# Optimization experiments

Hardware: AMD Instinct MI355X
Metric: run time of the kernel (lower is better)

The kernel has to match this reference:

```python
import jax, jax.numpy as jnp
import numpy as np
from jax import lax

H = 32  # hidden size


def _lstm_layer(x, Wih, Whh, bih, bhh):
    """x: [B, T, D_in]; returns [B, T, H]. PyTorch gate order i,f,g,o."""
    B = x.shape[0]
    b = bih + bhh  # [4H]
    # precompute input projections for all timesteps: [T, B, 4H]
    xp = jnp.einsum('btd,gd->tbg', x, Wih) + b

    def step(carry, xt):
        h, c = carry
        gates = xt + h @ Whh.T  # [B, 4H]
        i, f, g, o = jnp.split(gates, 4, axis=-1)
        i = jax.nn.sigmoid(i)
        f = jax.nn.sigmoid(f)
        g = jnp.tanh(g)
        o = jax.nn.sigmoid(o)
        c = f * c + i * g
        h = o * jnp.tanh(c)
        return (h, c), h

    init = (jnp.zeros((B, H), x.dtype), jnp.zeros((B, H), x.dtype))
    _, ys = lax.scan(step, init, xp)  # ys: [T, B, H]
    return jnp.swapaxes(ys, 0, 1)


def _lstm5(x, Wih0, Wih_rest, Whh, bih, bhh):
    h = _lstm_layer(x, Wih0, Whh[0], bih[0], bhh[0])
    for l in range(4):  # fixed small layer count
        h = _lstm_layer(h, Wih_rest[l], Whh[l + 1], bih[l + 1], bhh[l + 1])
    return h


def setup_inputs() -> dict:
    key = jax.random.key(0)
    ks = jax.random.split(key, 18)
    s = 1.0 / np.sqrt(H)
    B, T = 16384, 20
    u = lambda k, shp: jax.random.uniform(k, shp, jnp.float32, -s, s)
    return {
        'accel': jax.random.normal(ks[0], (B, T, 3), jnp.float32),
        'gyro': jax.random.normal(ks[1], (B, T, 3), jnp.float32),
        'accel_Wih0': u(ks[2], (4 * H, 3)),
        'accel_Wih_rest': u(ks[3], (4, 4 * H, H)),
        'accel_Whh': u(ks[4], (5, 4 * H, H)),
        'accel_bih': u(ks[5], (5, 4 * H)),
        'accel_bhh': u(ks[6], (5, 4 * H)),
        'gyro_Wih0': u(ks[7], (4 * H, 3)),
        'gyro_Wih_rest': u(ks[8], (4, 4 * H, H)),
        'gyro_Whh': u(ks[9], (5, 4 * H, H)),
        'gyro_bih': u(ks[10], (5, 4 * H)),
        'gyro_bhh': u(ks[11], (5, 4 * H)),
        'fc1_w': u(ks[12], (128, T * H * 2)),
        'fc1_b': u(ks[13], (128,)),
        'fc2_w': u(ks[14], (5, 128)),
        'fc2_b': u(ks[15], (5,)),
    }


def reference(accel, gyro, accel_Wih0, accel_Wih_rest, accel_Whh, accel_bih,
              accel_bhh, gyro_Wih0, gyro_Wih_rest, gyro_Whh, gyro_bih,
              gyro_bhh, fc1_w, fc1_b, fc2_w, fc2_b):
    a = _lstm5(accel, accel_Wih0, accel_Wih_rest, accel_Whh, accel_bih, accel_bhh)
    g = _lstm5(gyro, gyro_Wih0, gyro_Wih_rest, gyro_Whh, gyro_bih, gyro_bhh)
    x = jnp.concatenate([a, g], axis=1)          # [B, 2T, H]
    x = x.reshape(x.shape[0], -1)                # [B, 2*T*H]
    x = jax.nn.relu(x @ fc1_w.T + fc1_b)         # [B, 128]
    return x @ fc2_w.T + fc2_b                   # [B, 5]
```

## Files before the change

kernel.cpp:

```cpp
#include <hip/hip_runtime.h>
#include <math.h>

#define B_TOTAL 16384
#define T_STEPS 20
#define NGRP    1024

typedef __attribute__((ext_vector_type(8))) __bf16 bf16x8;
typedef __attribute__((ext_vector_type(4))) float f32x4;

__device__ __forceinline__ float sigf(float x) {
    return __builtin_amdgcn_rcpf(1.0f + __expf(-x));
}
__device__ __forceinline__ float tanhf_fast(float x) {
    return fmaf(-2.0f, __builtin_amdgcn_rcpf(__expf(2.0f * x) + 1.0f), 1.0f);
}

__device__ __forceinline__ __bf16 bf16_bits(unsigned short s) {
    __bf16 r; __builtin_memcpy(&r, &s, 2); return r;
}
__device__ __forceinline__ void split_trunc(float x, __bf16& hi, __bf16& lo) {
    unsigned u = __float_as_uint(x);
    hi = bf16_bits((unsigned short)(u >> 16));
    float l = x - __uint_as_float(u & 0xFFFF0000u);
    lo = bf16_bits((unsigned short)(__float_as_uint(l) >> 16));
}

__global__ __launch_bounds__(256, 4)
void lstm5_mfma(const float* __restrict__ accel, const float* __restrict__ gyro,
                const float* __restrict__ aWih0, const float* __restrict__ aWihR,
                const float* __restrict__ aWhh,  const float* __restrict__ aBih,
                const float* __restrict__ aBhh,
                const float* __restrict__ gWih0, const float* __restrict__ gWihR,
                const float* __restrict__ gWhh,  const float* __restrict__ gBih,
                const float* __restrict__ gBhh,
                __bf16* __restrict__ Xhi, __bf16* __restrict__ Xlo) {
    const int tid  = threadIdx.x;
    const int w    = tid >> 6;
    const int lane = tid & 63;
    const int e    = lane & 15;
    const int quad = lane >> 4;
    const int sensor = blockIdx.y;
    const int bbase  = blockIdx.x * 16;

    const float* xin  = sensor ? gyro  : accel;
    const float* Wih0 = sensor ? gWih0 : aWih0;
    const float* WihR = sensor ? gWihR : aWihR;
    const float* Whh  = sensor ? gWhh  : aWhh;
    const float* Bih  = sensor ? gBih  : aBih;
    const float* Bhh  = sensor ? gBhh  : aBhh;

    __shared__ __align__(16) __bf16 shi[20 * 512];
    __shared__ __align__(16) __bf16 slo[20 * 512];

    const int ug0 = w * 8 + quad;
    const int ug1 = w * 8 + 4 + quad;

    const int m_row   = lane & 15;
    const int orow_t0 = (m_row & 3) * 32 + (w * 8 + (m_row >> 2));
    const int orow_t1 = (m_row & 3) * 32 + (w * 8 + 4 + (m_row >> 2));

    bf16x8 wih_h0, wih_l0, wih_h1, wih_l1;
    bf16x8 whh_h0, whh_l0, whh_h1, whh_l1;
    f32x4  bias0v, bias1v;
    float  c0 = 0.f, c1 = 0.f;

#define LOAD_FRAG(Wsrc, orow, fh, fl)                         \
    {                                                         \
        const float* p_ = (Wsrc) + (orow) * 32 + quad * 8;    \
        _Pragma("unroll")                                     \
        for (int jj = 0; jj < 8; ++jj) {                      \
            __bf16 h_, l_;                                    \
            split_trunc(p_[jj], h_, l_);                      \
            (fh)[jj] = h_;  (fl)[jj] = l_;                    \
        }                                                     \
    }

#define LOAD_BIAS(l)                                                        \
    {                                                                       \
        _Pragma("unroll")                                                   \
        for (int r = 0; r < 4; ++r) {                                       \
            bias0v[r] = Bih[(l) * 128 + r * 32 + ug0] + Bhh[(l) * 128 + r * 32 + ug0]; \
            bias1v[r] = Bih[(l) * 128 + r * 32 + ug1] + Bhh[(l) * 128 + r * 32 + ug1]; \
        }                                                                   \
    }

#define ACT_STORE(t)                                                        \
    {                                                                       \
        float i0 = sigf(acc0[0]), f0 = sigf(acc0[1]);                       \
        float g0 = tanhf_fast(acc0[2]), o0 = sigf(acc0[3]);                 \
        c0 = f0 * c0 + i0 * g0;                                             \
        float h0 = o0 * tanhf_fast(c0);                                     \
        float i1 = sigf(acc1[0]), f1 = sigf(acc1[1]);                       \
        float g1 = tanhf_fast(acc1[2]), o1 = sigf(acc1[3]);                 \
        c1 = f1 * c1 + i1 * g1;                                             \
        float h1 = o1 * tanhf_fast(c1);                                     \
        __syncthreads();             \
        int i0x = (t) * 512 + w * 128 + e * 8 + quad;                       \
        int i1x = i0x + 4;                                                  \
        __bf16 hh_, ll_;                                                    \
        split_trunc(h0, hh_, ll_);  shi[i0x] = hh_;  slo[i0x] = ll_;        \
        split_trunc(h1, hh_, ll_);  shi[i1x] = hh_;  slo[i1x] = ll_;        \
        __syncthreads();       \
    }

    {
        LOAD_FRAG(Whh, orow_t0, whh_h0, whh_l0);
        LOAD_FRAG(Whh, orow_t1, whh_h1, whh_l1);
        LOAD_BIAS(0);
        float w0reg[2][4][3];
#pragma unroll
        for (int r = 0; r < 4; ++r)
#pragma unroll
            for (int k = 0; k < 3; ++k) {
                w0reg[0][r][k] = Wih0[(r * 32 + ug0) * 3 + k];
                w0reg[1][r][k] = Wih0[(r * 32 + ug1) * 3 + k];
            }
        const float* xrow = xin + (size_t)(bbase + e) * (T_STEPS * 3);

        for (int t = 0; t < T_STEPS; ++t) {
            float x0 = xrow[t * 3 + 0];
            float x1 = xrow[t * 3 + 1];
            float x2 = xrow[t * 3 + 2];
            f32x4 acc0 = bias0v;
            f32x4 acc1 = bias1v;
#pragma unroll
            for (int r = 0; r < 4; ++r) {
                acc0[r] = fmaf(w0reg[0][r][0], x0,
                          fmaf(w0reg[0][r][1], x1,
                          fmaf(w0reg[0][r][2], x2, acc0[r])));
                acc1[r] = fmaf(w0reg[1][r][0], x0,
                          fmaf(w0reg[1][r][1], x1,
                          fmaf(w0reg[1][r][2], x2, acc1[r])));
            }
            if (t > 0) {
                int rb = (t - 1) * 512 + quad * 128 + e * 8;
                bf16x8 bh = *(const bf16x8*)&shi[rb];
                bf16x8 bl = *(const bf16x8*)&slo[rb];
                acc0 = __builtin_amdgcn_mfma_f32_16x16x32_bf16(whh_h0, bh, acc0, 0, 0, 0);
                acc0 = __builtin_amdgcn_mfma_f32_16x16x32_bf16(whh_h0, bl, acc0, 0, 0, 0);
                acc0 = __builtin_amdgcn_mfma_f32_16x16x32_bf16(whh_l0, bh, acc0, 0, 0, 0);
                acc1 = __builtin_amdgcn_mfma_f32_16x16x32_bf16(whh_h1, bh, acc1, 0, 0, 0);
                acc1 = __builtin_amdgcn_mfma_f32_16x16x32_bf16(whh_h1, bl, acc1, 0, 0, 0);
                acc1 = __builtin_amdgcn_mfma_f32_16x16x32_bf16(whh_l1, bh, acc1, 0, 0, 0);
            }
            ACT_STORE(t);
        }
    }

    for (int l = 1; l < 5; ++l) {
        const float* Wi = WihR + (l - 1) * 4096;
        const float* Wh = Whh + l * 4096;
        LOAD_FRAG(Wi, orow_t0, wih_h0, wih_l0);
        LOAD_FRAG(Wi, orow_t1, wih_h1, wih_l1);
        LOAD_FRAG(Wh, orow_t0, whh_h0, whh_l0);
        LOAD_FRAG(Wh, orow_t1, whh_h1, whh_l1);
        LOAD_BIAS(l);
        c0 = 0.f; c1 = 0.f;

        for (int t = 0; t < T_STEPS; ++t) {
            f32x4 acc0, acc1;
            {
                int rb = t * 512 + quad * 128 + e * 8;
                bf16x8 bh = *(const bf16x8*)&shi[rb];
                bf16x8 bl = *(const bf16x8*)&slo[rb];
                acc0 = __builtin_amdgcn_mfma_f32_16x16x32_bf16(wih_h0, bh, bias0v, 0, 0, 0);
                acc0 = __builtin_amdgcn_mfma_f32_16x16x32_bf16(wih_h0, bl, acc0, 0, 0, 0);
                acc0 = __builtin_amdgcn_mfma_f32_16x16x32_bf16(wih_l0, bh, acc0, 0, 0, 0);
                acc1 = __builtin_amdgcn_mfma_f32_16x16x32_bf16(wih_h1, bh, bias1v, 0, 0, 0);
                acc1 = __builtin_amdgcn_mfma_f32_16x16x32_bf16(wih_h1, bl, acc1, 0, 0, 0);
                acc1 = __builtin_amdgcn_mfma_f32_16x16x32_bf16(wih_l1, bh, acc1, 0, 0, 0);
            }
            if (t > 0) {
                int rb = (t - 1) * 512 + quad * 128 + e * 8;
                bf16x8 bh = *(const bf16x8*)&shi[rb];
                bf16x8 bl = *(const bf16x8*)&slo[rb];
                acc0 = __builtin_amdgcn_mfma_f32_16x16x32_bf16(whh_h0, bh, acc0, 0, 0, 0);
                acc0 = __builtin_amdgcn_mfma_f32_16x16x32_bf16(whh_h0, bl, acc0, 0, 0, 0);
                acc0 = __builtin_amdgcn_mfma_f32_16x16x32_bf16(whh_l0, bh, acc0, 0, 0, 0);
                acc1 = __builtin_amdgcn_mfma_f32_16x16x32_bf16(whh_h1, bh, acc1, 0, 0, 0);
                acc1 = __builtin_amdgcn_mfma_f32_16x16x32_bf16(whh_h1, bl, acc1, 0, 0, 0);
                acc1 = __builtin_amdgcn_mfma_f32_16x16x32_bf16(whh_l1, bh, acc1, 0, 0, 0);
            }
            ACT_STORE(t);
        }
    }
    __syncthreads();

    {
        size_t base = ((size_t)(sensor * NGRP + blockIdx.x)) * (20 * 512);
        float4* dh = (float4*)(Xhi + base);
        float4* dl = (float4*)(Xlo + base);
        const float4* sh = (const float4*)shi;
        const float4* sl = (const float4*)slo;
        for (int i = tid; i < 20 * 512 / 8; i += 256) { dh[i] = sh[i]; dl[i] = sl[i]; }
    }
#undef LOAD_FRAG
#undef LOAD_BIAS
#undef ACT_STORE
}

__global__ void w1_prep(const float* __restrict__ w1,
                        __bf16* __restrict__ w1ah, __bf16* __restrict__ w1al) {
    int t = blockIdx.x * blockDim.x + threadIdx.x;
    if (t >= 20480) return;
    int lane = t & 63;
    int ks   = (t >> 6) % 40;
    int mt   = t / (64 * 40);
    int row  = mt * 16 + (lane & 15);
    int col0 = ks * 32 + (lane >> 4) * 8;
    const float* src = w1 + row * 1280 + col0;
#pragma unroll
    for (int j = 0; j < 8; ++j) {
        __bf16 h_, l_;
        split_trunc(src[j], h_, l_);
        w1ah[t * 8 + j] = h_;
        w1al[t * 8 + j] = l_;
    }
}

__global__ __launch_bounds__(256, 4)
void fc_mfma(const __bf16* __restrict__ Xhi, const __bf16* __restrict__ Xlo,
             const __bf16* __restrict__ w1ah, const __bf16* __restrict__ w1al,
             const float* __restrict__ fc1_b, const float* __restrict__ fc2_w,
             const float* __restrict__ fc2_b, float* __restrict__ out) {
    const int tid  = threadIdx.x;
    const int wv   = tid >> 6;
    const int lane = tid & 63;
    const int e    = lane & 15;
    const int quad = lane >> 4;
    const int g    = blockIdx.x;

    __shared__ __align__(16) f32x4 sacc[4][8][64];
    __shared__ float sred[4][16][5];

    f32x4 acc[8];
#pragma unroll
    for (int m = 0; m < 8; ++m) acc[m] = (f32x4){0.f, 0.f, 0.f, 0.f};

    for (int kk = 0; kk < 10; ++kk) {
        int ks = wv * 10 + kk;
        int sensor = ks / 20, t = ks % 20;
        size_t bb = ((size_t)(sensor * NGRP + g)) * (20 * 512) + t * 512 + lane * 8;
        bf16x8 bh = *(const bf16x8*)(Xhi + bb);
        bf16x8 bl = *(const bf16x8*)(Xlo + bb);
#pragma unroll
        for (int m = 0; m < 8; ++m) {
            const __bf16* ap = w1ah + ((size_t)((m * 40 + ks) * 64 + lane)) * 8;
            const __bf16* al = w1al + ((size_t)((m * 40 + ks) * 64 + lane)) * 8;
            bf16x8 ah = *(const bf16x8*)ap;
            bf16x8 av = *(const bf16x8*)al;
            acc[m] = __builtin_amdgcn_mfma_f32_16x16x32_bf16(ah, bh, acc[m], 0, 0, 0);
            acc[m] = __builtin_amdgcn_mfma_f32_16x16x32_bf16(ah, bl, acc[m], 0, 0, 0);
            acc[m] = __builtin_amdgcn_mfma_f32_16x16x32_bf16(av, bh, acc[m], 0, 0, 0);
        }
    }
#pragma unroll
    for (int m = 0; m < 8; ++m) sacc[wv][m][lane] = acc[m];
    __syncthreads();

    float p[5] = {0.f, 0.f, 0.f, 0.f, 0.f};
#pragma unroll
    for (int mm = 0; mm < 2; ++mm) {
        int mt = wv * 2 + mm;
        f32x4 z = sacc[0][mt][lane];
#pragma unroll
        for (int k = 1; k < 4; ++k) {
            f32x4 zz = sacc[k][mt][lane];
#pragma unroll
            for (int r = 0; r < 4; ++r) z[r] += zz[r];
        }
#pragma unroll
        for (int r = 0; r < 4; ++r) {
            int row = mt * 16 + quad * 4 + r;
            float v = fmaxf(z[r] + fc1_b[row], 0.f);
#pragma unroll
            for (int n = 0; n < 5; ++n) p[n] = fmaf(v, fc2_w[n * 128 + row], p[n]);
        }
    }
#pragma unroll
    for (int n = 0; n < 5; ++n) {
        p[n] += __shfl_xor(p[n], 16, 64);
        p[n] += __shfl_xor(p[n], 32, 64);
    }
    if (quad == 0) {
#pragma unroll
        for (int n = 0; n < 5; ++n) sred[wv][e][n] = p[n];
    }
    __syncthreads();
    if (tid < 80) {
        int col = tid / 5, n = tid - col * 5;
        out[(size_t)(g * 16 + col) * 5 + n] =
            sred[0][col][n] + sred[1][col][n] + sred[2][col][n] + sred[3][col][n] + fc2_b[n];
    }
}

extern "C" void kernel_launch(void* const* d_in, const int* in_sizes, int n_in,
                              void* d_out, int out_size, void* d_ws, size_t ws_size,
                              hipStream_t stream) {
    const float* accel  = (const float*)d_in[0];
    const float* gyro   = (const float*)d_in[1];
    const float* aWih0  = (const float*)d_in[2];
    const float* aWihR  = (const float*)d_in[3];
    const float* aWhh   = (const float*)d_in[4];
    const float* aBih   = (const float*)d_in[5];
    const float* aBhh   = (const float*)d_in[6];
    const float* gWih0  = (const float*)d_in[7];
    const float* gWihR  = (const float*)d_in[8];
    const float* gWhh   = (const float*)d_in[9];
    const float* gBih   = (const float*)d_in[10];
    const float* gBhh   = (const float*)d_in[11];
    const float* fc1_w  = (const float*)d_in[12];
    const float* fc1_b  = (const float*)d_in[13];
    const float* fc2_w  = (const float*)d_in[14];
    const float* fc2_b  = (const float*)d_in[15];
    float* out = (float*)d_out;

    const size_t XN = (size_t)2 * NGRP * 20 * 512;
    __bf16* Xhi  = (__bf16*)d_ws;
    __bf16* Xlo  = Xhi + XN;
    __bf16* W1ah = Xlo + XN;
    __bf16* W1al = W1ah + 163840;

    hipLaunchKernelGGL(w1_prep, dim3(80), dim3(256), 0, stream, fc1_w, W1ah, W1al);

    hipLaunchKernelGGL(lstm5_mfma, dim3(NGRP, 2), dim3(256), 0, stream,
                       accel, gyro, aWih0, aWihR, aWhh, aBih, aBhh,
                       gWih0, gWihR, gWhh, gBih, gBhh, Xhi, Xlo);

    hipLaunchKernelGGL(fc_mfma, dim3(NGRP), dim3(256), 0, stream,
                       Xhi, Xlo, W1ah, W1al, fc1_b, fc2_w, fc2_b, out);
}
```

Before: 294.4 us.

## Pack hidden-state stores with swizzled LDS layout, fuse gate math, batch FC groups

The activation math now shares the exponentials and reciprocals of all four gates, so each cell update uses two rcp calls instead of six. The hidden-state high/low bf16 values are packed as 32-bit words and written to an XOR-swizzled shared layout, with matching K-permutations in the weight fragments and the fc1 weight prep. This is meant to cut LDS store count and bank conflicts in the recurrent loop. The FC kernel now handles two batch groups per block, reusing each fc1 weight fragment load for twice as many MFMAs. The trade-offs are fewer FC blocks and a slightly different rounding path in the activations.

```diff
diff --git a/kernel.cpp b/kernel.cpp
--- a/kernel.cpp
+++ b/kernel.cpp
@@ -8,11 +8,12 @@
 typedef __attribute__((ext_vector_type(8))) __bf16 bf16x8;
 typedef __attribute__((ext_vector_type(4))) float f32x4;
 
-__device__ __forceinline__ float sigf(float x) {
-    return __builtin_amdgcn_rcpf(1.0f + __expf(-x));
-}
-__device__ __forceinline__ float tanhf_fast(float x) {
-    return fmaf(-2.0f, __builtin_amdgcn_rcpf(__expf(2.0f * x) + 1.0f), 1.0f);
+__device__ __forceinline__ unsigned pack_hi16(unsigned a, unsigned b) {
+#if __has_builtin(__builtin_amdgcn_perm)
+    return __builtin_amdgcn_perm(b, a, 0x07060302u);
+#else
+    return (a >> 16) | (b & 0xFFFF0000u);
+#endif
 }
 
 __device__ __forceinline__ __bf16 bf16_bits(unsigned short s) {
@@ -23,6 +24,20 @@
     hi = bf16_bits((unsigned short)(u >> 16));
     float l = x - __uint_as_float(u & 0xFFFF0000u);
     lo = bf16_bits((unsigned short)(__float_as_uint(l) >> 16));
+}
+
+__device__ __forceinline__ float lstm_act(f32x4 a, float& c) {
+    float eA = __expf(-a[0]);
+    float eB = __expf(-a[1]);
+    float eC = __expf(2.0f * a[2]);
+    float aA = 1.0f + eA, aB = 1.0f + eB, aC = 1.0f + eC;
+    float pAC = aA * aC;
+    float r1  = __builtin_amdgcn_rcpf(pAC * aB);
+    c = fmaf(c, pAC, (eC - 1.0f) * aB) * r1;
+    float eD = __expf(-a[3]);
+    float eE = __expf(2.0f * c);
+    float r2 = __builtin_amdgcn_rcpf((1.0f + eD) * (1.0f + eE));
+    return (eE - 1.0f) * r2;
 }
 
 __global__ __launch_bounds__(256, 4)
@@ -49,8 +64,13 @@
     const float* Bih  = sensor ? gBih  : aBih;
     const float* Bhh  = sensor ? gBhh  : aBhh;
 
-    __shared__ __align__(16) __bf16 shi[20 * 512];
-    __shared__ __align__(16) __bf16 slo[20 * 512];
+    __shared__ __align__(16) unsigned shi[20 * 256];
+    __shared__ __align__(16) unsigned slo[20 * 256];
+    const __bf16* sh16 = (const __bf16*)shi;
+    const __bf16* sl16 = (const __bf16*)slo;
+
+    const int wr_idx  = w * 64 + ((e * 4) ^ (w << 3)) + quad;
+    const int rb_base = quad * 128 + ((e * 8) ^ (quad << 4));
 
     const int ug0 = w * 8 + quad;
     const int ug1 = w * 8 + 4 + quad;
@@ -70,7 +90,7 @@
         _Pragma("unroll")                                     \
         for (int jj = 0; jj < 8; ++jj) {                      \
             __bf16 h_, l_;                                    \
-            split_trunc(p_[jj], h_, l_);                      \
+            split_trunc(p_[(jj >> 1) + ((jj & 1) << 2)], h_, l_); \
             (fh)[jj] = h_;  (fl)[jj] = l_;                    \
         }                                                     \
     }
@@ -86,20 +106,16 @@
 
 #define ACT_STORE(t)                                                        \
     {                                                                       \
-        float i0 = sigf(acc0[0]), f0 = sigf(acc0[1]);                       \
-        float g0 = tanhf_fast(acc0[2]), o0 = sigf(acc0[3]);                 \
-        c0 = f0 * c0 + i0 * g0;                                             \
-        float h0 = o0 * tanhf_fast(c0);                                     \
-        float i1 = sigf(acc1[0]), f1 = sigf(acc1[1]);                       \
-        float g1 = tanhf_fast(acc1[2]), o1 = sigf(acc1[3]);                 \
-        c1 = f1 * c1 + i1 * g1;                                             \
-        float h1 = o1 * tanhf_fast(c1);                                     \
+        float h0 = lstm_act(acc0, c0);                                      \
+        float h1 = lstm_act(acc1, c1);                                      \
+        unsigned b0 = __float_as_uint(h0), b1 = __float_as_uint(h1);        \
+        unsigned hp = pack_hi16(b0, b1);                                    \
+        float l0 = h0 - __uint_as_float(b0 & 0xFFFF0000u);                  \
+        float l1 = h1 - __uint_as_float(b1 & 0xFFFF0000u);                  \
+        unsigned lp = pack_hi16(__float_as_uint(l0), __float_as_uint(l1));  \
         __syncthreads();             \
-        int i0x = (t) * 512 + w * 128 + e * 8 + quad;                       \
-        int i1x = i0x + 4;                                                  \
-        __bf16 hh_, ll_;                                                    \
-        split_trunc(h0, hh_, ll_);  shi[i0x] = hh_;  slo[i0x] = ll_;        \
-        split_trunc(h1, hh_, ll_);  shi[i1x] = hh_;  slo[i1x] = ll_;        \
+        shi[(t) * 256 + wr_idx] = hp;                                       \
+        slo[(t) * 256 + wr_idx] = lp;                                       \
         __syncthreads();       \
     }
 
@@ -133,9 +149,9 @@
                           fmaf(w0reg[1][r][2], x2, acc1[r])));
             }
             if (t > 0) {
-                int rb = (t - 1) * 512 + quad * 128 + e * 8;
-                bf16x8 bh = *(const bf16x8*)&shi[rb];
-                bf16x8 bl = *(const bf16x8*)&slo[rb];
+                int rb = (t - 1) * 512 + rb_base;
+                bf16x8 bh = *(const bf16x8*)(sh16 + rb);
+                bf16x8 bl = *(const bf16x8*)(sl16 + rb);
                 acc0 = __builtin_amdgcn_mfma_f32_16x16x32_bf16(whh_h0, bh, acc0, 0, 0, 0);
                 acc0 = __builtin_amdgcn_mfma_f32_16x16x32_bf16(whh_h0, bl, acc0, 0, 0, 0);
                 acc0 = __builtin_amdgcn_mfma_f32_16x16x32_bf16(whh_l0, bh, acc0, 0, 0, 0);
@@ -158,22 +174,20 @@
         c0 = 0.f; c1 = 0.f;
 
         for (int t = 0; t < T_STEPS; ++t) {
+            const int rb1 = t * 512 + rb_base;
+            bf16x8 bh1 = *(const bf16x8*)(sh16 + rb1);
+            bf16x8 bl1 = *(const bf16x8*)(sl16 + rb1);
             f32x4 acc0, acc1;
-            {
-                int rb = t * 512 + quad * 128 + e * 8;
-                bf16x8 bh = *(const bf16x8*)&shi[rb];
-                bf16x8 bl = *(const bf16x8*)&slo[rb];
-                acc0 = __builtin_amdgcn_mfma_f32_16x16x32_bf16(wih_h0, bh, bias0v, 0, 0, 0);
-                acc0 = __builtin_amdgcn_mfma_f32_16x16x32_bf16(wih_h0, bl, acc0, 0, 0, 0);
-                acc0 = __builtin_amdgcn_mfma_f32_16x16x32_bf16(wih_l0, bh, acc0, 0, 0, 0);
-                acc1 = __builtin_amdgcn_mfma_f32_16x16x32_bf16(wih_h1, bh, bias1v, 0, 0, 0);
-                acc1 = __builtin_amdgcn_mfma_f32_16x16x32_bf16(wih_h1, bl, acc1, 0, 0, 0);
-                acc1 = __builtin_amdgcn_mfma_f32_16x16x32_bf16(wih_l1, bh, acc1, 0, 0, 0);
-            }
+            acc0 = __builtin_amdgcn_mfma_f32_16x16x32_bf16(wih_h0, bh1, bias0v, 0, 0, 0);
+            acc0 = __builtin_amdgcn_mfma_f32_16x16x32_bf16(wih_h0, bl1, acc0, 0, 0, 0);
+            acc0 = __builtin_amdgcn_mfma_f32_16x16x32_bf16(wih_l0, bh1, acc0, 0, 0, 0);
+            acc1 = __builtin_amdgcn_mfma_f32_16x16x32_bf16(wih_h1, bh1, bias1v, 0, 0, 0);
+            acc1 = __builtin_amdgcn_mfma_f32_16x16x32_bf16(wih_h1, bl1, acc1, 0, 0, 0);
+            acc1 = __builtin_amdgcn_mfma_f32_16x16x32_bf16(wih_l1, bh1, acc1, 0, 0, 0);
             if (t > 0) {
-                int rb = (t - 1) * 512 + quad * 128 + e * 8;
-                bf16x8 bh = *(const bf16x8*)&shi[rb];
-                bf16x8 bl = *(const bf16x8*)&slo[rb];
+                const int rb0 = rb1 - 512;
+                bf16x8 bh = *(const bf16x8*)(sh16 + rb0);
+                bf16x8 bl = *(const bf16x8*)(sl16 + rb0);
                 acc0 = __builtin_amdgcn_mfma_f32_16x16x32_bf16(whh_h0, bh, acc0, 0, 0, 0);
                 acc0 = __builtin_amdgcn_mfma_f32_16x16x32_bf16(whh_h0, bl, acc0, 0, 0, 0);
                 acc0 = __builtin_amdgcn_mfma_f32_16x16x32_bf16(whh_l0, bh, acc0, 0, 0, 0);
@@ -192,7 +206,7 @@
         float4* dl = (float4*)(Xlo + base);
         const float4* sh = (const float4*)shi;
         const float4* sl = (const float4*)slo;
-        for (int i = tid; i < 20 * 512 / 8; i += 256) { dh[i] = sh[i]; dl[i] = sl[i]; }
+        for (int i = tid; i < 1280; i += 256) { dh[i] = sh[i]; dl[i] = sl[i]; }
     }
 #undef LOAD_FRAG
 #undef LOAD_BIAS
@@ -212,7 +226,7 @@
 #pragma unroll
     for (int j = 0; j < 8; ++j) {
         __bf16 h_, l_;
-        split_trunc(src[j], h_, l_);
+        split_trunc(src[(j >> 1) + ((j & 1) << 2)], h_, l_);
         w1ah[t * 8 + j] = h_;
         w1al[t * 8 + j] = l_;
     }
@@ -228,69 +242,83 @@
     const int lane = tid & 63;
     const int e    = lane & 15;
     const int quad = lane >> 4;
-    const int g    = blockIdx.x;
+    const int g0   = blockIdx.x * 2;
+
+    const int lnoff = (lane * 8) ^ (quad << 4);
 
     __shared__ __align__(16) f32x4 sacc[4][8][64];
     __shared__ float sred[4][16][5];
 
-    f32x4 acc[8];
-#pragma unroll
-    for (int m = 0; m < 8; ++m) acc[m] = (f32x4){0.f, 0.f, 0.f, 0.f};
+    f32x4 acc[2][8];
+#pragma unroll
+    for (int p = 0; p < 2; ++p)
+#pragma unroll
+        for (int m = 0; m < 8; ++m) acc[p][m] = (f32x4){0.f, 0.f, 0.f, 0.f};
 
     for (int kk = 0; kk < 10; ++kk) {
         int ks = wv * 10 + kk;
         int sensor = ks / 20, t = ks % 20;
-        size_t bb = ((size_t)(sensor * NGRP + g)) * (20 * 512) + t * 512 + lane * 8;
-        bf16x8 bh = *(const bf16x8*)(Xhi + bb);
-        bf16x8 bl = *(const bf16x8*)(Xlo + bb);
+        size_t bb0 = ((size_t)(sensor * NGRP + g0)) * (20 * 512) + t * 512 + lnoff;
+        size_t bb1 = bb0 + (size_t)(20 * 512);
+        bf16x8 bh0 = *(const bf16x8*)(Xhi + bb0);
+        bf16x8 bl0 = *(const bf16x8*)(Xlo + bb0);
+        bf16x8 bh1 = *(const bf16x8*)(Xhi + bb1);
+        bf16x8 bl1 = *(const bf16x8*)(Xlo + bb1);
 #pragma unroll
         for (int m = 0; m < 8; ++m) {
             const __bf16* ap = w1ah + ((size_t)((m * 40 + ks) * 64 + lane)) * 8;
             const __bf16* al = w1al + ((size_t)((m * 40 + ks) * 64 + lane)) * 8;
             bf16x8 ah = *(const bf16x8*)ap;
             bf16x8 av = *(const bf16x8*)al;
-            acc[m] = __builtin_amdgcn_mfma_f32_16x16x32_bf16(ah, bh, acc[m], 0, 0, 0);
-            acc[m] = __builtin_amdgcn_mfma_f32_16x16x32_bf16(ah, bl, acc[m], 0, 0, 0);
-            acc[m] = __builtin_amdgcn_mfma_f32_16x16x32_bf16(av, bh, acc[m], 0, 0, 0);
-        }
-    }
-#pragma unroll
-    for (int m = 0; m < 8; ++m) sacc[wv][m][lane] = acc[m];
-    __syncthreads();
-
-    float p[5] = {0.f, 0.f, 0.f, 0.f, 0.f};
-#pragma unroll
-    for (int mm = 0; mm < 2; ++mm) {
-        int mt = wv * 2 + mm;
-        f32x4 z = sacc[0][mt][lane];
-#pragma unroll
-        for (int k = 1; k < 4; ++k) {
-            f32x4 zz = sacc[k][mt][lane];
-#pragma unroll
-            for (int r = 0; r < 4; ++r) z[r] += zz[r];
-        }
-#pragma unroll
-        for (int r = 0; r < 4; ++r) {
-            int row = mt * 16 + quad * 4 + r;
-            float v = fmaxf(z[r] + fc1_b[row], 0.f);
-#pragma unroll
-            for (int n = 0; n < 5; ++n) p[n] = fmaf(v, fc2_w[n * 128 + row], p[n]);
-        }
-    }
-#pragma unroll
-    for (int n = 0; n < 5; ++n) {
-        p[n] += __shfl_xor(p[n], 16, 64);
-        p[n] += __shfl_xor(p[n], 32, 64);
-    }
-    if (quad == 0) {
-#pragma unroll
-        for (int n = 0; n < 5; ++n) sred[wv][e][n] = p[n];
-    }
-    __syncthreads();
-    if (tid < 80) {
-        int col = tid / 5, n = tid - col * 5;
-        out[(size_t)(g * 16 + col) * 5 + n] =
-            sred[0][col][n] + sred[1][col][n] + sred[2][col][n] + sred[3][col][n] + fc2_b[n];
+            acc[0][m] = __builtin_amdgcn_mfma_f32_16x16x32_bf16(ah, bh0, acc[0][m], 0, 0, 0);
+            acc[0][m] = __builtin_amdgcn_mfma_f32_16x16x32_bf16(ah, bl0, acc[0][m], 0, 0, 0);
+            acc[0][m] = __builtin_amdgcn_mfma_f32_16x16x32_bf16(av, bh0, acc[0][m], 0, 0, 0);
+            acc[1][m] = __builtin_amdgcn_mfma_f32_16x16x32_bf16(ah, bh1, acc[1][m], 0, 0, 0);
+            acc[1][m] = __builtin_amdgcn_mfma_f32_16x16x32_bf16(ah, bl1, acc[1][m], 0, 0, 0);
+            acc[1][m] = __builtin_amdgcn_mfma_f32_16x16x32_bf16(av, bh1, acc[1][m], 0, 0, 0);
+        }
+    }
+
+#pragma unroll 2
+    for (int grp = 0; grp < 2; ++grp) {
+#pragma unroll
+        for (int m = 0; m < 8; ++m) sacc[wv][m][lane] = acc[grp][m];
+        __syncthreads();
+
+        float p[5] = {0.f, 0.f, 0.f, 0.f, 0.f};
+#pragma unroll
+        for (int mm = 0; mm < 2; ++mm) {
+            int mt = wv * 2 + mm;
+            f32x4 z = sacc[0][mt][lane];
+#pragma unroll
+            for (int k = 1; k < 4; ++k) {
+                f32x4 zz = sacc[k][mt][lane];
+#pragma unroll
+                for (int r = 0; r < 4; ++r) z[r] += zz[r];
+            }
+#pragma unroll
+            for (int r = 0; r < 4; ++r) {
+                int row = mt * 16 + quad * 4 + r;
+                float v = fmaxf(z[r] + fc1_b[row], 0.f);
+#pragma unroll
+                for (int n = 0; n < 5; ++n) p[n] = fmaf(v, fc2_w[n * 128 + row], p[n]);
+            }
+        }
+#pragma unroll
+        for (int n = 0; n < 5; ++n) {
+            p[n] += __shfl_xor(p[n], 16, 64);
+            p[n] += __shfl_xor(p[n], 32, 64);
+        }
+        if (quad == 0) {
+#pragma unroll
+            for (int n = 0; n < 5; ++n) sred[wv][e][n] = p[n];
+        }
+        __syncthreads();
+        if (tid < 80) {
+            int col = tid / 5, n = tid - col * 5;
+            out[(size_t)((g0 + grp) * 16 + col) * 5 + n] =
+                sred[0][col][n] + sred[1][col][n] + sred[2][col][n] + sred[3][col][n] + fc2_b[n];
+        }
     }
 }
 
@@ -327,6 +355,6 @@
                        accel, gyro, aWih0, aWihR, aWhh, aBih, aBhh,
                        gWih0, gWihR, gWhh, gBih, gBhh, Xhi, Xlo);
 
-    hipLaunchKernelGGL(fc_mfma, dim3(NGRP), dim3(256), 0, stream,
+    hipLaunchKernelGGL(fc_mfma, dim3(NGRP / 2), dim3(256), 0, stream,
                        Xhi, Xlo, W1ah, W1al, fc1_b, fc2_w, fc2_b, out);
 }
```

Result: slower. 302.7 us (+2.8%).

## Use 512-thread LSTM blocks with one gate tile per wave and swizzled LDS

Applied to the files above, without the earlier changes.

The LSTM kernel now uses 8 waves per block, each handling one 16-unit gate tile instead of two. This halves per-thread work and register use on the serial recurrence and raises occupancy. The gate activations are merged into a fused lstm_act that needs fewer reciprocals. The hidden-state layout in shared memory is XOR-swizzled to cut bank conflicts, and the FC kernel's read index is changed to match. The trade-off is more threads synchronising at each __syncthreads per timestep, and the merged activation formula may behave differently when the exponentials overflow.

```diff
diff --git a/kernel.cpp b/kernel.cpp
--- a/kernel.cpp
+++ b/kernel.cpp
@@ -7,13 +7,6 @@
 
 typedef __attribute__((ext_vector_type(8))) __bf16 bf16x8;
 typedef __attribute__((ext_vector_type(4))) float f32x4;
-
-__device__ __forceinline__ float sigf(float x) {
-    return __builtin_amdgcn_rcpf(1.0f + __expf(-x));
-}
-__device__ __forceinline__ float tanhf_fast(float x) {
-    return fmaf(-2.0f, __builtin_amdgcn_rcpf(__expf(2.0f * x) + 1.0f), 1.0f);
-}
 
 __device__ __forceinline__ __bf16 bf16_bits(unsigned short s) {
     __bf16 r; __builtin_memcpy(&r, &s, 2); return r;
@@ -25,7 +18,21 @@
     lo = bf16_bits((unsigned short)(__float_as_uint(l) >> 16));
 }
 
-__global__ __launch_bounds__(256, 4)
+__device__ __forceinline__ float lstm_act(f32x4 a, float& c) {
+    float eA = __expf(-a[0]);
+    float eB = __expf(-a[1]);
+    float eC = __expf(2.0f * a[2]);
+    float aA = 1.0f + eA, aB = 1.0f + eB, aC = 1.0f + eC;
+    float pAC = aA * aC;
+    float r1  = __builtin_amdgcn_rcpf(pAC * aB);
+    c = fmaf(c, pAC, (eC - 1.0f) * aB) * r1;
+    float eD = __expf(-a[3]);
+    float eE = __expf(2.0f * c);
+    float r2 = __builtin_amdgcn_rcpf((1.0f + eD) * (1.0f + eE));
+    return (eE - 1.0f) * r2;
+}
+
+__global__ __launch_bounds__(512, 8)
 void lstm5_mfma(const float* __restrict__ accel, const float* __restrict__ gyro,
                 const float* __restrict__ aWih0, const float* __restrict__ aWihR,
                 const float* __restrict__ aWhh,  const float* __restrict__ aBih,
@@ -52,19 +59,20 @@
     __shared__ __align__(16) __bf16 shi[20 * 512];
     __shared__ __align__(16) __bf16 slo[20 * 512];
 
-    const int ug0 = w * 8 + quad;
-    const int ug1 = w * 8 + 4 + quad;
-
-    const int m_row   = lane & 15;
-    const int orow_t0 = (m_row & 3) * 32 + (w * 8 + (m_row >> 2));
-    const int orow_t1 = (m_row & 3) * 32 + (w * 8 + 4 + (m_row >> 2));
-
-    bf16x8 wih_h0, wih_l0, wih_h1, wih_l1;
-    bf16x8 whh_h0, whh_l0, whh_h1, whh_l1;
-    f32x4  bias0v, bias1v;
-    float  c0 = 0.f, c1 = 0.f;
-
-#define LOAD_FRAG(Wsrc, orow, fh, fl)                         \
+    const int ug  = w * 4 + quad;
+    const int swz = (e >> 1) & 3;
+
+    const int widx = (e * 16 + ((w * 2 + (quad >> 1)) ^ (swz << 2))) * 2 + (quad & 1);
+    const int rb_base = e * 32 + ((quad ^ swz) << 3);
+
+    const int m_row = lane & 15;
+    const int orow  = (m_row & 3) * 32 + (w * 4 + (m_row >> 2));
+
+    bf16x8 wih_h, wih_l, whh_h, whh_l;
+    f32x4  biasv;
+    float  c0 = 0.f;
+
+#define LOAD_FRAG(Wsrc, fh, fl)                               \
     {                                                         \
         const float* p_ = (Wsrc) + (orow) * 32 + quad * 8;    \
         _Pragma("unroll")                                     \
@@ -78,70 +86,49 @@
 #define LOAD_BIAS(l)                                                        \
     {                                                                       \
         _Pragma("unroll")                                                   \
-        for (int r = 0; r < 4; ++r) {                                       \
-            bias0v[r] = Bih[(l) * 128 + r * 32 + ug0] + Bhh[(l) * 128 + r * 32 + ug0]; \
-            bias1v[r] = Bih[(l) * 128 + r * 32 + ug1] + Bhh[(l) * 128 + r * 32 + ug1]; \
-        }                                                                   \
+        for (int r = 0; r < 4; ++r)                                         \
+            biasv[r] = Bih[(l) * 128 + r * 32 + ug] + Bhh[(l) * 128 + r * 32 + ug]; \
     }
 
 #define ACT_STORE(t)                                                        \
     {                                                                       \
-        float i0 = sigf(acc0[0]), f0 = sigf(acc0[1]);                       \
-        float g0 = tanhf_fast(acc0[2]), o0 = sigf(acc0[3]);                 \
-        c0 = f0 * c0 + i0 * g0;                                             \
-        float h0 = o0 * tanhf_fast(c0);                                     \
-        float i1 = sigf(acc1[0]), f1 = sigf(acc1[1]);                       \
-        float g1 = tanhf_fast(acc1[2]), o1 = sigf(acc1[3]);                 \
-        c1 = f1 * c1 + i1 * g1;                                             \
-        float h1 = o1 * tanhf_fast(c1);                                     \
+        float h0 = lstm_act(acc, c0);                                       \
+        __bf16 hh_, ll_;                                                    \
+        split_trunc(h0, hh_, ll_);                                          \
         __syncthreads();             \
-        int i0x = (t) * 512 + w * 128 + e * 8 + quad;                       \
-        int i1x = i0x + 4;                                                  \
-        __bf16 hh_, ll_;                                                    \
-        split_trunc(h0, hh_, ll_);  shi[i0x] = hh_;  slo[i0x] = ll_;        \
-        split_trunc(h1, hh_, ll_);  shi[i1x] = hh_;  slo[i1x] = ll_;        \
+        shi[(t) * 512 + widx] = hh_;                                        \
+        slo[(t) * 512 + widx] = ll_;                                        \
         __syncthreads();       \
     }
 
     {
-        LOAD_FRAG(Whh, orow_t0, whh_h0, whh_l0);
-        LOAD_FRAG(Whh, orow_t1, whh_h1, whh_l1);
+        LOAD_FRAG(Whh, whh_h, whh_l);
         LOAD_BIAS(0);
-        float w0reg[2][4][3];
+        float w0reg[4][3];
 #pragma unroll
         for (int r = 0; r < 4; ++r)
 #pragma unroll
-            for (int k = 0; k < 3; ++k) {
-                w0reg[0][r][k] = Wih0[(r * 32 + ug0) * 3 + k];
-                w0reg[1][r][k] = Wih0[(r * 32 + ug1) * 3 + k];
-            }
+            for (int k = 0; k < 3; ++k)
+                w0reg[r][k] = Wih0[(r * 32 + ug) * 3 + k];
         const float* xrow = xin + (size_t)(bbase + e) * (T_STEPS * 3);
 
         for (int t = 0; t < T_STEPS; ++t) {
             float x0 = xrow[t * 3 + 0];
             float x1 = xrow[t * 3 + 1];
             float x2 = xrow[t * 3 + 2];
-            f32x4 acc0 = bias0v;
-            f32x4 acc1 = bias1v;
-#pragma unroll
-            for (int r = 0; r < 4; ++r) {
-                acc0[r] = fmaf(w0reg[0][r][0], x0,
-                          fmaf(w0reg[0][r][1], x1,
-                          fmaf(w0reg[0][r][2], x2, acc0[r])));
-                acc1[r] = fmaf(w0reg[1][r][0], x0,
-                          fmaf(w0reg[1][r][1], x1,
-                          fmaf(w0reg[1][r][2], x2, acc1[r])));
-            }
+            f32x4 acc = biasv;
+#pragma unroll
+            for (int r = 0; r < 4; ++r)
+                acc[r] = fmaf(w0reg[r][0], x0,
+                         fmaf(w0reg[r][1], x1,
+                         fmaf(w0reg[r][2], x2, acc[r])));
             if (t > 0) {
-                int rb = (t - 1) * 512 + quad * 128 + e * 8;
+                int rb = (t - 1) * 512 + rb_base;
                 bf16x8 bh = *(const bf16x8*)&shi[rb];
                 bf16x8 bl = *(const bf16x8*)&slo[rb];
-                acc0 = __builtin_amdgcn_mfma_f32_16x16x32_bf16(whh_h0, bh, acc0, 0, 0, 0);
-                acc0 = __builtin_amdgcn_mfma_f32_16x16x32_bf16(whh_h0, bl, acc0, 0, 0, 0);
-                acc0 = __builtin_amdgcn_mfma_f32_16x16x32_bf16(whh_l0, bh, acc0, 0, 0, 0);
-                acc1 = __builtin_amdgcn_mfma_f32_16x16x32_bf16(whh_h1, bh, acc1, 0, 0, 0);
-                acc1 = __builtin_amdgcn_mfma_f32_16x16x32_bf16(whh_h1, bl, acc1, 0, 0, 0);
-                acc1 = __builtin_amdgcn_mfma_f32_16x16x32_bf16(whh_l1, bh, acc1, 0, 0, 0);
+                acc = __builtin_amdgcn_mfma_f32_16x16x32_bf16(whh_h, bh, acc, 0, 0, 0);
+                acc = __builtin_amdgcn_mfma_f32_16x16x32_bf16(whh_h, bl, acc, 0, 0, 0);
+                acc = __builtin_amdgcn_mfma_f32_16x16x32_bf16(whh_l, bh, acc, 0, 0, 0);
             }
             ACT_STORE(t);
         }
@@ -150,36 +137,26 @@
     for (int l = 1; l < 5; ++l) {
         const float* Wi = WihR + (l - 1) * 4096;
         const float* Wh = Whh + l * 4096;
-        LOAD_FRAG(Wi, orow_t0, wih_h0, wih_l0);
-        LOAD_FRAG(Wi, orow_t1, wih_h1, wih_l1);
-        LOAD_FRAG(Wh, orow_t0, whh_h0, whh_l0);
-        LOAD_FRAG(Wh, orow_t1, whh_h1, whh_l1);
+        LOAD_FRAG(Wi, wih_h, wih_l);
+        LOAD_FRAG(Wh, whh_h, whh_l);
         LOAD_BIAS(l);
-        c0 = 0.f; c1 = 0.f;
+        c0 = 0.f;
 
         for (int t = 0; t < T_STEPS; ++t) {
-            f32x4 acc0, acc1;
-            {
-                int rb = t * 512 + quad * 128 + e * 8;
-                bf16x8 bh = *(const bf16x8*)&shi[rb];
-                bf16x8 bl = *(const bf16x8*)&slo[rb];
-                acc0 = __builtin_amdgcn_mfma_f32_16x16x32_bf16(wih_h0, bh, bias0v, 0, 0, 0);
-                acc0 = __builtin_amdgcn_mfma_f32_16x16x32_bf16(wih_h0, bl, acc0, 0, 0, 0);
-                acc0 = __builtin_amdgcn_mfma_f32_16x16x32_bf16(wih_l0, bh, acc0, 0, 0, 0);
-                acc1 = __builtin_amdgcn_mfma_f32_16x16x32_bf16(wih_h1, bh, bias1v, 0, 0, 0);
-                acc1 = __builtin_amdgcn_mfma_f32_16x16x32_bf16(wih_h1, bl, acc1, 0, 0, 0);
-                acc1 = __builtin_amdgcn_mfma_f32_16x16x32_bf16(wih_l1, bh, acc1, 0, 0, 0);
-            }
+            const int rb1 = t * 512 + rb_base;
+            bf16x8 bh1 = *(const bf16x8*)&shi[rb1];
+            bf16x8 bl1 = *(const bf16x8*)&slo[rb1];
+            f32x4 acc;
+            acc = __builtin_amdgcn_mfma_f32_16x16x32_bf16(wih_h, bh1, biasv, 0, 0, 0);
+            acc = __builtin_amdgcn_mfma_f32_16x16x32_bf16(wih_h, bl1, acc, 0, 0, 0);
+            acc = __builtin_amdgcn_mfma_f32_16x16x32_bf16(wih_l, bh1, acc, 0, 0, 0);
             if (t > 0) {
-                int rb = (t - 1) * 512 + quad * 128 + e * 8;
-                bf16x8 bh = *(const bf16x8*)&shi[rb];
-                bf16x8 bl = *(const bf16x8*)&slo[rb];
-                acc0 = __builtin_amdgcn_mfma_f32_16x16x32_bf16(whh_h0, bh, acc0, 0, 0, 0);
-                acc0 = __builtin_amdgcn_mfma_f32_16x16x32_bf16(whh_h0, bl, acc0, 0, 0, 0);
-                acc0 = __builtin_amdgcn_mfma_f32_16x16x32_bf16(whh_l0, bh, acc0, 0, 0, 0);
-                acc1 = __builtin_amdgcn_mfma_f32_16x16x32_bf16(whh_h1, bh, acc1, 0, 0, 0);
-                acc1 = __builtin_amdgcn_mfma_f32_16x16x32_bf16(whh_h1, bl, acc1, 0, 0, 0);
-                acc1 = __builtin_amdgcn_mfma_f32_16x16x32_bf16(whh_l1, bh, acc1, 0, 0, 0);
+                const int rb0 = rb1 - 512;
+                bf16x8 bh = *(const bf16x8*)&shi[rb0];
+                bf16x8 bl = *(const bf16x8*)&slo[rb0];
+                acc = __builtin_amdgcn_mfma_f32_16x16x32_bf16(whh_h, bh, acc, 0, 0, 0);
+                acc = __builtin_amdgcn_mfma_f32_16x16x32_bf16(whh_h, bl, acc, 0, 0, 0);
+                acc = __builtin_amdgcn_mfma_f32_16x16x32_bf16(whh_l, bh, acc, 0, 0, 0);
             }
             ACT_STORE(t);
         }
@@ -192,7 +169,7 @@
         float4* dl = (float4*)(Xlo + base);
         const float4* sh = (const float4*)shi;
         const float4* sl = (const float4*)slo;
-        for (int i = tid; i < 20 * 512 / 8; i += 256) { dh[i] = sh[i]; dl[i] = sl[i]; }
+        for (int i = tid; i < 1280; i += 512) { dh[i] = sh[i]; dl[i] = sl[i]; }
     }
 #undef LOAD_FRAG
 #undef LOAD_BIAS
@@ -230,6 +207,8 @@
     const int quad = lane >> 4;
     const int g    = blockIdx.x;
 
+    const int lnoff = e * 32 + ((quad ^ ((e >> 1) & 3)) << 3);
+
     __shared__ __align__(16) f32x4 sacc[4][8][64];
     __shared__ float sred[4][16][5];
 
@@ -240,7 +219,7 @@
     for (int kk = 0; kk < 10; ++kk) {
         int ks = wv * 10 + kk;
         int sensor = ks / 20, t = ks % 20;
-        size_t bb = ((size_t)(sensor * NGRP + g)) * (20 * 512) + t * 512 + lane * 8;
+        size_t bb = ((size_t)(sensor * NGRP + g)) * (20 * 512) + t * 512 + lnoff;
         bf16x8 bh = *(const bf16x8*)(Xhi + bb);
         bf16x8 bl = *(const bf16x8*)(Xlo + bb);
 #pragma unroll
@@ -323,7 +302,7 @@
 
     hipLaunchKernelGGL(w1_prep, dim3(80), dim3(256), 0, stream, fc1_w, W1ah, W1al);
 
-    hipLaunchKernelGGL(lstm5_mfma, dim3(NGRP, 2), dim3(256), 0, stream,
+    hipLaunchKernelGGL(lstm5_mfma, dim3(NGRP, 2), dim3(512), 0, stream,
                        accel, gyro, aWih0, aWihR, aWhh, aBih, aBhh,
                        gWih0, gWihR, gWhh, gBih, gBhh, Xhi, Xlo);
 
```

Result: no change. 291.2 us (-1.1%).
